# Optimization experiments

Hardware: AMD Instinct MI355X
Metric: run time of the kernel (lower is better)

Reference implementation:

```python
import jax, jax.numpy as jnp
import numpy as np

V_PATCH_NUMS = (1, 2, 3, 4, 5, 6, 8, 10, 13, 16)


def _pool_matrix(in_size: int, out_size: int) -> jnp.ndarray:
    # Matrix form of torch adaptive_avg_pool1d (== F.interpolate mode='area'):
    # window i averages input bins [floor(i*in/out), ceil((i+1)*in/out)).
    M = np.zeros((out_size, in_size), dtype=np.float32)
    for i in range(out_size):
        s = (i * in_size) // out_size
        e = -((-(i + 1) * in_size) // out_size)  # ceil division
        M[i, s:e] = 1.0 / (e - s)
    return jnp.asarray(M)


def setup_inputs() -> dict:
    key = jax.random.key(0)
    k1, k2 = jax.random.split(key)
    B, C, H, W = 64, 32, 16, 16
    vocab = 4096
    f = jax.random.normal(k1, (B, C, H, W), dtype=jnp.float32)
    # embedding init: uniform(-1/vocab, 1/vocab), as in the torch module
    emb = (jax.random.uniform(k2, (vocab, C), dtype=jnp.float32) * 2.0 - 1.0) / vocab
    return {"f": f, "emb": emb}


def reference(f, emb):
    # Multi-scale residual VQ: per scale -> area-downsample residual,
    # nearest-codebook argmin, embedding gather, bicubic-upsample,
    # accumulate into f_hat and subtract from f_rest.
    B, C, H, W = f.shape
    f = jax.lax.stop_gradient(f)            # f_no_grad in torch
    x = jnp.transpose(f, (0, 2, 3, 1))      # BHWC for resize/gather
    f_rest = x
    f_hat = jnp.zeros_like(x)
    emb_ng = jax.lax.stop_gradient(emb)     # distances use embedding.weight.data
    e_sq = jnp.sum(emb_ng * emb_ng, axis=1)  # [vocab]
    SN = len(V_PATCH_NUMS)
    for si, pn in enumerate(V_PATCH_NUMS):
        last = si == SN - 1
        if last:
            z = f_rest                       # [B,H,W,C]
        else:
            Mh = _pool_matrix(H, pn)
            Mw = _pool_matrix(W, pn)
            z = jnp.einsum('ph,qw,bhwc->bpqc', Mh, Mw, f_rest)  # area interp
        z_NC = z.reshape(-1, C)
        # squared L2 distance to every code: ||z||^2 + ||e||^2 - 2 z e^T
        d = jnp.sum(z_NC * z_NC, axis=1, keepdims=True) + e_sq - 2.0 * (z_NC @ emb_ng.T)
        idx = jnp.argmin(d, axis=1).reshape(B, pn, pn)
        h = emb[idx]                         # [B,pn,pn,C] gather (grad-carrying emb)
        if not last:
            h = jax.image.resize(h, (B, H, W, C), method='cubic')  # bicubic up
        f_hat = f_hat + h
        f_rest = f_rest - h
    return jnp.transpose(f_hat, (0, 3, 1, 2))  # back to BCHW
```

## Files before the change

### kernel.cpp

```cpp
#include <hip/hip_runtime.h>
#include <math.h>

#define WS_ESQ   0
#define WS_STATE 4096
#define WS_FHAT  (4096 + 524288)
#define WS_Z     (4096 + 2*524288)
#define WS_PSC   (4096 + 3*524288)
#define WS_PIX   (4096 + 3*524288 + 131072)

__device__ __forceinline__ float4 v4add(float4 a, float4 b) {
    return make_float4(__fadd_rn(a.x,b.x), __fadd_rn(a.y,b.y),
                       __fadd_rn(a.z,b.z), __fadd_rn(a.w,b.w));
}
__device__ __forceinline__ float4 v4sq(float4 a) {
    return make_float4(__fmul_rn(a.x,a.x), __fmul_rn(a.y,a.y),
                       __fmul_rn(a.z,a.z), __fmul_rn(a.w,a.w));
}
__device__ __forceinline__ float np_pw32(float4 q0, float4 q1, float4 q2, float4 q3,
                                         float4 q4, float4 q5, float4 q6, float4 q7) {
    float4 rA = v4add(v4add(v4add(q0, q2), q4), q6);
    float4 rB = v4add(v4add(v4add(q1, q3), q5), q7);
    float l = __fadd_rn(__fadd_rn(rA.x, rA.y), __fadd_rn(rA.z, rA.w));
    float h = __fadd_rn(__fadd_rn(rB.x, rB.y), __fadd_rn(rB.z, rB.w));
    return __fadd_rn(l, h);
}

__device__ __forceinline__ double keys64(double x) {
    if (x < 1.0)      return ((1.5*x - 2.5)*x)*x + 1.0;
    else if (x < 2.0) return ((-0.5*x + 2.5)*x - 4.0)*x + 2.0;
    return 0.0;
}

__global__ __launch_bounds__(256) void vq_apply(
    const float* __restrict__ f, const float* __restrict__ emb,
    float* __restrict__ esq, float* __restrict__ state, float* __restrict__ fhat,
    float* __restrict__ zws, const float* __restrict__ psc, const int* __restrict__ pix,
    int sIdx, int pn, int pnPrev, int ncbPrev)
{
    __shared__ float fr[1280];
    __shared__ float hs[676];
    __shared__ int   idx_arr[176];
    __shared__ float U[256];
    __shared__ float red_f[1360];
    __shared__ int   red_i[1360];

    const int tid = threadIdx.x;
    const int wg  = blockIdx.x;
    if (wg >= 512) {
        int j = ((wg - 512) << 8) + tid;
        const float4* e4 = (const float4*)(emb + (size_t)j*32);
        esq[j] = np_pw32(v4sq(e4[0]),v4sq(e4[1]),v4sq(e4[2]),v4sq(e4[3]),
                         v4sq(e4[4]),v4sq(e4[5]),v4sq(e4[6]),v4sq(e4[7]));
        return;
    }
    const int b  = wg >> 3;
    const int c0 = (wg & 7) * 4;

    const float* src = (sIdx <= 1) ? f : state;
    for (int o = tid; o < 1024; o += 256) {
        int cc = o >> 8, yx = o & 255;
        fr[yx*5 + cc] = src[b*8192 + (c0 + cc)*256 + yx];
    }
    __syncthreads();

    if (sIdx > 0) {
        const int Vp = pnPrev * pnPrev;
        const int step = ncbPrev >> 3;
        for (int t = tid; t < Vp*8; t += 256) {
            int v = t >> 3, k = t & 7;
            const size_t base = (size_t)((v << 6) + b) * ncbPrev;
            float best = INFINITY; int bi = 0;
            for (int ch = k*step; ch < (k+1)*step; ++ch) {
                float sc = psc[base + ch];
                if (sc < best) { best = sc; bi = pix[base + ch]; }
            }
            red_f[t] = best; red_i[t] = bi;
        }
        __syncthreads();
        if (tid < Vp) {
            float best = INFINITY; int bi = 0;
            for (int k = 0; k < 8; ++k) {
                float sc = red_f[tid*8 + k];
                if (sc < best) { best = sc; bi = red_i[tid*8 + k]; }
            }
            idx_arr[tid] = bi;
        }
        __syncthreads();
        for (int t = tid; t < Vp*4; t += 256)
            hs[t] = emb[(size_t)idx_arr[t >> 2]*32 + c0 + (t & 3)];
        if (tid < 16) {
            double scl = 16.0 / (double)pnPrev;
            double inv = 1.0 / scl;
            double sp = ((double)tid + 0.5) * inv - 0.5;
            double w64[16]; double tot = 0.0;
            for (int q = 0; q < pnPrev; ++q) {
                double wv = keys64(fabs(sp - (double)q));
                w64[q] = wv; tot += wv;
            }
            for (int q = 0; q < pnPrev; ++q) U[tid*16 + q] = (float)(w64[q] / tot);
        }
        __syncthreads();
        {
            const double inv = 1.0 / (16.0 / (double)pnPrev);
            const int yx = tid, y = yx >> 4, x = yx & 15;
            double sy = ((double)y + 0.5) * inv - 0.5;
            double sx = ((double)x + 0.5) * inv - 0.5;
            int p0 = (int)floor(sy) - 1, q0 = (int)floor(sx) - 1;
            int pa = max(0, p0), pb = min(pnPrev - 1, p0 + 3);
            int qa = max(0, q0), qb = min(pnPrev - 1, q0 + 3);
            float acc0 = 0.f, acc1 = 0.f, acc2 = 0.f, acc3 = 0.f;
            for (int p = pa; p <= pb; ++p) {
                float wy = U[y*16 + p];
                for (int q = qa; q <= qb; ++q) {
                    float wx = U[x*16 + q];
                    const float* hp = &hs[(p*pnPrev + q)*4];
                    acc0 = __fadd_rn(acc0, __fmul_rn(__fmul_rn(hp[0], wy), wx));
                    acc1 = __fadd_rn(acc1, __fmul_rn(__fmul_rn(hp[1], wy), wx));
                    acc2 = __fadd_rn(acc2, __fmul_rn(__fmul_rn(hp[2], wy), wx));
                    acc3 = __fadd_rn(acc3, __fmul_rn(__fmul_rn(hp[3], wy), wx));
                }
            }
            float a4[4] = {acc0, acc1, acc2, acc3};
            #pragma unroll
            for (int cc = 0; cc < 4; ++cc) {
                float frv = __fsub_rn(fr[yx*5 + cc], a4[cc]);
                fr[yx*5 + cc] = frv;
                int go = b*8192 + (c0 + cc)*256 + yx;
                state[go] = frv;
                fhat[go] = (sIdx == 1) ? a4[cc] : __fadd_rn(fhat[go], a4[cc]);
            }
        }
        __syncthreads();
    }

    const int V = pn * pn;
    if (pn < 16) {
        if (tid < V) {
            int p = tid / pn, q = tid - p*pn;
            int sh = (p*16)/pn, eh = ((p+1)*16 + pn - 1)/pn;
            int sw = (q*16)/pn, ew = ((q+1)*16 + pn - 1)/pn;
            float Mh = (float)(1.0/(double)(eh - sh));
            float Mw = (float)(1.0/(double)(ew - sw));
            float coef = __fmul_rn(Mh, Mw);
            float a4[4] = {0.f, 0.f, 0.f, 0.f};
            for (int hh = sh; hh < eh; ++hh)
                for (int wy = sw; wy < ew; ++wy) {
                    const float* fp = &fr[(hh*16 + wy)*5];
                    #pragma unroll
                    for (int cc = 0; cc < 4; ++cc)
                        a4[cc] = __fadd_rn(a4[cc], __fmul_rn(coef, fp[cc]));
                }
            *(float4*)(zws + (size_t)((tid << 6) + b)*32 + c0) =
                make_float4(a4[0], a4[1], a4[2], a4[3]);
        }
    } else {
        const int yx = tid;
        *(float4*)(zws + (size_t)((yx << 6) + b)*32 + c0) =
            make_float4(fr[yx*5], fr[yx*5 + 1], fr[yx*5 + 2], fr[yx*5 + 3]);
    }
}

typedef float f32x16 __attribute__((ext_vector_type(16)));
typedef float f32x2  __attribute__((ext_vector_type(2)));

#define SLOADW2(E0, E1, F0, F1, Q2, JS) { \
    const float* _pe = emb + ((size_t)(JS) << 5); \
    const float* _pq = esq + (JS); \
    asm volatile("s_load_dwordx16 %0, %5, 0x0\n\t" \
                 "s_load_dwordx16 %1, %5, 0x40\n\t" \
                 "s_load_dwordx16 %2, %5, 0x80\n\t" \
                 "s_load_dwordx16 %3, %5, 0xC0\n\t" \
                 "s_load_dwordx2  %4, %6, 0x0\n\t" \
                 "s_waitcnt lgkmcnt(0)" \
        : "=&s"(E0), "=&s"(E1), "=&s"(F0), "=&s"(F1), "=&s"(Q2) \
        : "s"(_pe), "s"(_pq)); }

#define DOT4S(EV, K, ZA, ZB) { \
    const float ex_ = EV[4*(K)+0], ey_ = EV[4*(K)+1]; \
    const float ez_ = EV[4*(K)+2], ew_ = EV[4*(K)+3]; \
    acc0 = __fmaf_rn(ex_, ZA.x, acc0); acc1 = __fmaf_rn(ex_, ZB.x, acc1); \
    acc0 = __fmaf_rn(ey_, ZA.y, acc0); acc1 = __fmaf_rn(ey_, ZB.y, acc1); \
    acc0 = __fmaf_rn(ez_, ZA.z, acc0); acc1 = __fmaf_rn(ez_, ZB.z, acc1); \
    acc0 = __fmaf_rn(ew_, ZA.w, acc0); acc1 = __fmaf_rn(ew_, ZB.w, acc1); }

#define CODE_STEP(E0, E1, SQ, J) { \
    float acc0 = 0.f, acc1 = 0.f; \
    DOT4S(E0, 0, a0, b0) DOT4S(E0, 1, a1, b1) DOT4S(E0, 2, a2, b2) DOT4S(E0, 3, a3, b3) \
    DOT4S(E1, 0, a4, b4) DOT4S(E1, 1, a5, b5) DOT4S(E1, 2, a6, b6) DOT4S(E1, 3, a7, b7) \
    float d0 = __fsub_rn(__fadd_rn(zsq0, SQ), __fmul_rn(2.0f, acc0)); \
    float d1 = __fsub_rn(__fadd_rn(zsq1, SQ), __fmul_rn(2.0f, acc1)); \
    if (d0 < best0) { best0 = d0; bi0 = (J); } \
    if (d1 < best1) { best1 = d1; bi1 = (J); } }

__global__ __launch_bounds__(256, 4) void vq_scan(
    const float* __restrict__ emb, const float* __restrict__ esq,
    const float* __restrict__ zws, float* __restrict__ psc, int* __restrict__ pix,
    int V, int ncbMask, int PB, int CB)
{
    __shared__ float red_f[512];
    __shared__ int   red_i[512];

    const int tid  = threadIdx.x;
    const int cb   = blockIdx.x / PB;
    const int pblk = blockIdx.x - cb * PB;
    const int w    = tid >> 6, lane = tid & 63;
    const int N    = V << 6;

    const int pair0 = (pblk << 7) + lane;
    const int p0c = min(pair0, N - 1), p1c = min(pair0 + 64, N - 1);
    const float4* za = (const float4*)(zws + (size_t)p0c*32);
    const float4* zb = (const float4*)(zws + (size_t)p1c*32);
    float4 a0 = za[0], a1 = za[1], a2 = za[2], a3 = za[3];
    float4 a4 = za[4], a5 = za[5], a6 = za[6], a7 = za[7];
    float4 b0 = zb[0], b1 = zb[1], b2 = zb[2], b3 = zb[3];
    float4 b4 = zb[4], b5 = zb[5], b6 = zb[6], b7 = zb[7];
    float zsq0 = np_pw32(v4sq(a0),v4sq(a1),v4sq(a2),v4sq(a3),
                         v4sq(a4),v4sq(a5),v4sq(a6),v4sq(a7));
    float zsq1 = np_pw32(v4sq(b0),v4sq(b1),v4sq(b2),v4sq(b3),
                         v4sq(b4),v4sq(b5),v4sq(b6),v4sq(b7));

    const int jchunk = cb * CB;
    const int pw     = CB >> 2;
    const int w_u    = __builtin_amdgcn_readfirstlane(w);
    const int jbase  = jchunk + w_u * pw;

    float best0 = INFINITY, best1 = INFINITY; int bi0 = 0, bi1 = 0;
    for (int i = 0; i < pw; i += 2) {
        const int j = jbase + i;
        f32x16 e0, e1, f0, f1; f32x2 q2;
        SLOADW2(e0, e1, f0, f1, q2, j);
        const float q0 = q2[0], q1 = q2[1];
        CODE_STEP(e0, e1, q0, j);
        CODE_STEP(f0, f1, q1, j + 1);
    }

    red_f[w*128 + lane]      = best0;  red_i[w*128 + lane]      = bi0;
    red_f[w*128 + 64 + lane] = best1;  red_i[w*128 + 64 + lane] = bi1;
    __syncthreads();

    if (tid < 128) {
        const int p = (pblk << 7) + tid;
        if (p < N) {
            float bb = INFINITY; int bi = 0x7fffffff;
            #pragma unroll
            for (int ww = 0; ww < 4; ++ww) {
                float sc = red_f[ww*128 + tid];
                int   ji = red_i[ww*128 + tid];
                if (sc < bb || (sc == bb && ji < bi)) { bb = sc; bi = ji; }
            }
            psc[(size_t)p*(ncbMask + 1) + cb] = bb;
            pix[(size_t)p*(ncbMask + 1) + cb] = bi;
        }
    }
}

__global__ __launch_bounds__(256) void vq_final(
    const float* __restrict__ emb, const float* __restrict__ fhat,
    const float* __restrict__ psc, const int* __restrict__ pix,
    float* __restrict__ out)
{
    __shared__ int idx_arr[256];
    const int tid = threadIdx.x;
    const int b = blockIdx.x;
    {
        float best = INFINITY; int bi = 0;
        const size_t pb0 = (size_t)((tid << 6) + b) * 8;
        for (int ch = 0; ch < 8; ++ch) {
            float sc = psc[pb0 + ch];
            if (sc < best) { best = sc; bi = pix[pb0 + ch]; }
        }
        idx_arr[tid] = bi;
    }
    __syncthreads();
    for (int o = tid; o < 8192; o += 256) {
        int c = o >> 8, yx = o & 255;
        out[b*8192 + o] = __fadd_rn(fhat[(size_t)b*8192 + o],
                                    emb[(size_t)idx_arr[yx]*32 + c]);
    }
}

extern "C" void kernel_launch(void* const* d_in, const int* in_sizes, int n_in,
                              void* d_out, int out_size, void* d_ws, size_t ws_size,
                              hipStream_t stream) {
    const float* f   = (const float*)d_in[0];
    const float* emb = (const float*)d_in[1];
    float* ws  = (float*)d_ws;
    float* out = (float*)d_out;
    float* esq   = ws + WS_ESQ;
    float* state = ws + WS_STATE;
    float* fhatp = ws + WS_FHAT;
    float* zws   = ws + WS_Z;
    float* psc   = ws + WS_PSC;
    int*   pixp  = (int*)(ws + WS_PIX);
    static const int pns[10]  = {1, 2, 3, 4, 5, 6, 8, 10, 13, 16};
    static const int ncbl[10] = {7, 7, 6, 6, 5, 5, 4, 4, 3, 3};

    for (int s = 0; s < 10; ++s) {
        int pn = pns[s], V = pn*pn, sh = ncbl[s];
        int PB = ((V << 6) + 127) >> 7;
        vq_apply<<<(s == 0) ? 528 : 512, 256, 0, stream>>>(
            f, emb, esq, state, fhatp, zws, psc, pixp,
            s, pn, s > 0 ? pns[s-1] : 0, s > 0 ? (1 << ncbl[s-1]) : 0);
        vq_scan<<<PB << sh, 256, 0, stream>>>(emb, esq, zws, psc, pixp,
                                              V, (1 << sh) - 1, PB, 4096 >> sh);
    }
    vq_final<<<64, 256, 0, stream>>>(emb, fhatp, psc, pixp, out);
}
```

Baseline: 389.7 us.

## Replace partial-result buffers with packed 64-bit atomicMin argmin keys

Each scan block now packs its best distance (converted to an order-preserving unsigned integer) and code index into one 64-bit key and reduces it with a global atomicMin. This replaces writing per-chunk score and index arrays that the next apply kernel and the final kernel had to re-reduce. Keys live in double-buffered arrays that the apply kernel resets. The codebook chunk sizes per scale also change, which changes how many scan blocks launch. Tie-breaking by lowest index is kept by the key ordering, and atomic contention rises when many chunks target the same pixel.

```diff
diff --git a/kernel.cpp b/kernel.cpp
--- a/kernel.cpp
+++ b/kernel.cpp
@@ -6,7 +6,6 @@
 #define WS_FHAT  (4096 + 524288)
 #define WS_Z     (4096 + 2*524288)
 #define WS_PSC   (4096 + 3*524288)
-#define WS_PIX   (4096 + 3*524288 + 131072)
 
 __device__ __forceinline__ float4 v4add(float4 a, float4 b) {
     return make_float4(__fadd_rn(a.x,b.x), __fadd_rn(a.y,b.y),
@@ -34,15 +33,14 @@
 __global__ __launch_bounds__(256) void vq_apply(
     const float* __restrict__ f, const float* __restrict__ emb,
     float* __restrict__ esq, float* __restrict__ state, float* __restrict__ fhat,
-    float* __restrict__ zws, const float* __restrict__ psc, const int* __restrict__ pix,
-    int sIdx, int pn, int pnPrev, int ncbPrev)
+    float* __restrict__ zws, const unsigned long long* __restrict__ keysPrev,
+    unsigned long long* __restrict__ keysCur,
+    int sIdx, int pn, int pnPrev)
 {
     __shared__ float fr[1280];
     __shared__ float hs[676];
     __shared__ int   idx_arr[176];
     __shared__ float U[256];
-    __shared__ float red_f[1360];
-    __shared__ int   red_i[1360];
 
     const int tid = threadIdx.x;
     const int wg  = blockIdx.x;
@@ -56,6 +54,11 @@
     const int b  = wg >> 3;
     const int c0 = (wg & 7) * 4;
 
+    if ((wg & 7) == 0) {
+        const int V = pn * pn;
+        for (int v = tid; v < V; v += 256) keysCur[(v << 6) + b] = ~0ull;
+    }
+
     const float* src = (sIdx <= 1) ? f : state;
     for (int o = tid; o < 1024; o += 256) {
         int cc = o >> 8, yx = o & 255;
@@ -65,26 +68,8 @@
 
     if (sIdx > 0) {
         const int Vp = pnPrev * pnPrev;
-        const int step = ncbPrev >> 3;
-        for (int t = tid; t < Vp*8; t += 256) {
-            int v = t >> 3, k = t & 7;
-            const size_t base = (size_t)((v << 6) + b) * ncbPrev;
-            float best = INFINITY; int bi = 0;
-            for (int ch = k*step; ch < (k+1)*step; ++ch) {
-                float sc = psc[base + ch];
-                if (sc < best) { best = sc; bi = pix[base + ch]; }
-            }
-            red_f[t] = best; red_i[t] = bi;
-        }
-        __syncthreads();
-        if (tid < Vp) {
-            float best = INFINITY; int bi = 0;
-            for (int k = 0; k < 8; ++k) {
-                float sc = red_f[tid*8 + k];
-                if (sc < best) { best = sc; bi = red_i[tid*8 + k]; }
-            }
-            idx_arr[tid] = bi;
-        }
+        if (tid < Vp)
+            idx_arr[tid] = (int)(keysPrev[((size_t)tid << 6) + b] & 0xffffffffu);
         __syncthreads();
         for (int t = tid; t < Vp*4; t += 256)
             hs[t] = emb[(size_t)idx_arr[t >> 2]*32 + c0 + (t & 3)];
@@ -194,8 +179,8 @@
 
 __global__ __launch_bounds__(256, 4) void vq_scan(
     const float* __restrict__ emb, const float* __restrict__ esq,
-    const float* __restrict__ zws, float* __restrict__ psc, int* __restrict__ pix,
-    int V, int ncbMask, int PB, int CB)
+    const float* __restrict__ zws, unsigned long long* __restrict__ keys,
+    int V, int PB, int CB)
 {
     __shared__ float red_f[512];
     __shared__ int   red_i[512];
@@ -248,29 +233,24 @@
                 int   ji = red_i[ww*128 + tid];
                 if (sc < bb || (sc == bb && ji < bi)) { bb = sc; bi = ji; }
             }
-            psc[(size_t)p*(ncbMask + 1) + cb] = bb;
-            pix[(size_t)p*(ncbMask + 1) + cb] = bi;
+            unsigned u  = __float_as_uint(bb);
+            unsigned mu = (u & 0x80000000u) ? ~u : (u | 0x80000000u);
+            unsigned long long key =
+                ((unsigned long long)mu << 32) | (unsigned long long)(unsigned)bi;
+            atomicMin(&keys[p], key);
         }
     }
 }
 
 __global__ __launch_bounds__(256) void vq_final(
     const float* __restrict__ emb, const float* __restrict__ fhat,
-    const float* __restrict__ psc, const int* __restrict__ pix,
+    const unsigned long long* __restrict__ keys,
     float* __restrict__ out)
 {
     __shared__ int idx_arr[256];
     const int tid = threadIdx.x;
     const int b = blockIdx.x;
-    {
-        float best = INFINITY; int bi = 0;
-        const size_t pb0 = (size_t)((tid << 6) + b) * 8;
-        for (int ch = 0; ch < 8; ++ch) {
-            float sc = psc[pb0 + ch];
-            if (sc < best) { best = sc; bi = pix[pb0 + ch]; }
-        }
-        idx_arr[tid] = bi;
-    }
+    idx_arr[tid] = (int)(keys[((size_t)tid << 6) + b] & 0xffffffffu);
     __syncthreads();
     for (int o = tid; o < 8192; o += 256) {
         int c = o >> 8, yx = o & 255;
@@ -290,19 +270,20 @@
     float* state = ws + WS_STATE;
     float* fhatp = ws + WS_FHAT;
     float* zws   = ws + WS_Z;
-    float* psc   = ws + WS_PSC;
-    int*   pixp  = (int*)(ws + WS_PIX);
-    static const int pns[10]  = {1, 2, 3, 4, 5, 6, 8, 10, 13, 16};
-    static const int ncbl[10] = {7, 7, 6, 6, 5, 5, 4, 4, 3, 3};
+    unsigned long long* keysA = (unsigned long long*)(ws + WS_PSC);
+    static const int pns[10] = {1, 2, 3, 4, 5, 6, 8, 10, 13, 16};
+    static const int cbs[10] = {16, 16, 16, 16, 32, 32, 64, 128, 128, 256};
 
     for (int s = 0; s < 10; ++s) {
-        int pn = pns[s], V = pn*pn, sh = ncbl[s];
+        int pn = pns[s], V = pn*pn, CB = cbs[s];
+        int NC = 4096 / CB;
         int PB = ((V << 6) + 127) >> 7;
+        unsigned long long* keysCur  = keysA + (size_t)(s & 1) * 16384;
+        unsigned long long* keysPrev = keysA + (size_t)((s & 1) ^ 1) * 16384;
         vq_apply<<<(s == 0) ? 528 : 512, 256, 0, stream>>>(
-            f, emb, esq, state, fhatp, zws, psc, pixp,
-            s, pn, s > 0 ? pns[s-1] : 0, s > 0 ? (1 << ncbl[s-1]) : 0);
-        vq_scan<<<PB << sh, 256, 0, stream>>>(emb, esq, zws, psc, pixp,
-                                              V, (1 << sh) - 1, PB, 4096 >> sh);
-    }
-    vq_final<<<64, 256, 0, stream>>>(emb, fhatp, psc, pixp, out);
-}
+            f, emb, esq, state, fhatp, zws, keysPrev, keysCur,
+            s, pn, s > 0 ? pns[s-1] : 0);
+        vq_scan<<<PB * NC, 256, 0, stream>>>(emb, esq, zws, keysCur, V, PB, CB);
+    }
+    vq_final<<<64, 256, 0, stream>>>(emb, fhatp, keysA + 16384, out);
+}
```

After: 368.1 us (median of 2 runs). 5.5% less time.
